# Performance work log

Measured on AMD Instinct MI355X. Metric: run time of the kernel, lower is better.

The kernel has to match this reference:

```python
import jax, jax.numpy as jnp
import numpy as np

EPS = 1e-5

def _bn_train(x, gamma, beta):
    # BatchNorm2d in training mode: batch stats over (N,H,W), biased variance
    mean = jnp.mean(x, axis=(0, 2, 3), keepdims=True)
    var = jnp.mean((x - mean) ** 2, axis=(0, 2, 3), keepdims=True)
    xn = (x - mean) / jnp.sqrt(var + EPS)
    return xn * gamma[None, :, None, None] + beta[None, :, None, None]

def _bin_act(x):
    # forward: sign(x); backward: grad of clamp(x,-1,1) (STE)
    c = jnp.clip(x, -1.0, 1.0)
    return jax.lax.stop_gradient(jnp.sign(x) - c) + c

def _bin_conv(x, w_flat, out_chn, in_chn, k=3, stride=1, padding=1):
    w = w_flat.reshape(out_chn, in_chn, k, k)
    scale = jax.lax.stop_gradient(jnp.mean(jnp.abs(w), axis=(1, 2, 3), keepdims=True))
    cw = jnp.clip(w, -1.0, 1.0)
    bw = jax.lax.stop_gradient(scale * jnp.sign(w) - cw) + cw
    return jax.lax.conv_general_dilated(
        x, bw, window_strides=(stride, stride),
        padding=[(padding, padding), (padding, padding)],
        dimension_numbers=('NCHW', 'OIHW', 'NCHW'))

def _prelu(x, a):
    return jnp.where(x >= 0, x, a * x)

def setup_inputs() -> dict:
    key = jax.random.key(0)
    ks = jax.random.split(key, 4)
    C = 128
    x = jax.random.normal(ks[0], (64, C, 56, 56), dtype=jnp.float32)
    # HardBinaryConv stores weights as (n,1); init small, mixed-sign
    w1 = (jax.random.uniform(ks[1], (C * C * 9, 1), dtype=jnp.float32) - 0.5) * 0.002
    w2 = (jax.random.uniform(ks[2], (C * C * 9, 1), dtype=jnp.float32) - 0.5) * 0.002
    ones = jnp.ones((C,), jnp.float32)
    zeros = jnp.zeros((C,), jnp.float32)
    a = jnp.float32(0.25)
    return {
        'x': x,
        'bn1_g': ones, 'bn1_b': zeros,
        'w1': w1, 'prelu1_a': a,
        'bn2_g': ones, 'bn2_b': zeros,
        'w2': w2, 'prelu2_a': a,
        'bn3_g': ones, 'bn3_b': zeros,
        'prelu3_a': a,
    }

def reference(x, bn1_g, bn1_b, w1, prelu1_a, bn2_g, bn2_b, w2, prelu2_a, bn3_g, bn3_b, prelu3_a):
    C = x.shape[1]
    out = _bn_train(x, bn1_g, bn1_b)
    out = _bin_act(out)
    out = _prelu(_bin_conv(out, w1, C, C), prelu1_a)
    out = _bn_train(out, bn2_g, bn2_b)
    out = _bin_act(out)
    out = _bin_conv(out, w2, C, C)
    out = _prelu(out, prelu2_a)
    out = _bn_train(out, bn3_g, bn3_b)
    out = out + x  # identity shortcut (stride=1, in_planes==planes)
    out = _prelu(out, prelu3_a)
    return out
```

## Files before the change

kernel.cpp:

```cpp
#include <hip/hip_runtime.h>
#include <hip/hip_bf16.h>

typedef __attribute__((ext_vector_type(8))) short short8;
typedef __attribute__((ext_vector_type(4))) int i32x4;

#define HW     3136
#define M_TOT  200704
#define NSTEP  18
#define NBLK   1568

__device__ __forceinline__ void gload_lds16(const void* g, void* l) {
    __builtin_amdgcn_global_load_lds(
        (const __attribute__((address_space(1))) void*)g,
        (__attribute__((address_space(3))) void*)l, 16, 0, 0);
}

__global__ __launch_bounds__(256) void wsign_kernel(const float* __restrict__ w1,
                                                    const float* __restrict__ w2,
                                                    char* __restrict__ ws1,
                                                    char* __restrict__ ws2) {
    int i = blockIdx.x * 256 + threadIdx.x;
    const float* w = w1;
    char* wsz = ws1;
    if (i >= 147456) { i -= 147456; w = w2; wsz = ws2; }
    int e = i & 15, l = (i >> 4) & 63, f = (i >> 10) & 7, s = i >> 13;
    int cout = f * 16 + (l & 15);
    int k = s * 64 + (l >> 4) * 16 + e;
    int tap = k >> 7, cin = k & 127;
    float v = w[(cout * 128 + cin) * 9 + tap];
    wsz[i] = v > 0.f ? (char)1 : (v < 0.f ? (char)-1 : (char)0);
}

__global__ __launch_bounds__(256) void wscale_kernel(const float* __restrict__ w1,
                                                     const float* __restrict__ w2,
                                                     float* __restrict__ scale1,
                                                     float* __restrict__ scale2) {
    int o = blockIdx.x;
    const float* w = w1;
    float* scale = scale1;
    if (o >= 128) { o -= 128; w = w2; scale = scale2; }
    int t = threadIdx.x;
    float s = 0.f;
    for (int i = t; i < 1152; i += 256) s += fabsf(w[o * 1152 + i]);
    __shared__ float r1[256];
    r1[t] = s; __syncthreads();
    for (int off = 128; off > 0; off >>= 1) {
        if (t < off) r1[t] += r1[t + off];
        __syncthreads();
    }
    if (t == 0) scale[o] = r1[0] * (1.f / 1152.f);
}

__global__ __launch_bounds__(256) void stats_nchw_kernel(const float* __restrict__ x,
                                                         float* __restrict__ psum,
                                                         float* __restrict__ psq) {
    int bid = blockIdx.x;
    int n = bid >> 7, c = bid & 127;
    const float* p = x + (n * 128 + c) * HW;
    int t = threadIdx.x;
    float s = 0.f, q = 0.f;
    for (int i = t; i < HW; i += 256) { float v = p[i]; s += v; q += v * v; }
    __shared__ float r1[256], r2[256];
    r1[t] = s; r2[t] = q; __syncthreads();
    for (int off = 128; off > 0; off >>= 1) {
        if (t < off) { r1[t] += r1[t + off]; r2[t] += r2[t + off]; }
        __syncthreads();
    }
    if (t == 0) { psum[c * 64 + n] = r1[0]; psq[c * 64 + n] = r2[0]; }
}

__global__ void finalize_kernel(const float* __restrict__ psum, const float* __restrict__ psq,
                                int P, float* __restrict__ mean, float* __restrict__ rstd) {
    int c = threadIdx.x;
    if (c >= 128) return;
    float s = 0.f, q = 0.f;
    for (int j = 0; j < P; ++j) { s += psum[c * P + j]; q += psq[c * P + j]; }
    const float invN = 1.f / 200704.f;
    float m = s * invN;
    float var = q * invN - m * m;
    mean[c] = m;
    rstd[c] = 1.f / sqrtf(var + 1e-5f);
}

__global__ __launch_bounds__(256) void finalizeB_kernel(const float* __restrict__ psumB,
                                                        const float* __restrict__ psqB,
                                                        float* __restrict__ mean,
                                                        float* __restrict__ rstd) {
    int c = blockIdx.x, t = threadIdx.x;
    float s = 0.f, q = 0.f;
    for (int j = t; j < NBLK; j += 256) { s += psumB[c * NBLK + j]; q += psqB[c * NBLK + j]; }
    __shared__ float r1[256], r2[256];
    r1[t] = s; r2[t] = q; __syncthreads();
    for (int off = 128; off > 0; off >>= 1) {
        if (t < off) { r1[t] += r1[t + off]; r2[t] += r2[t + off]; }
        __syncthreads();
    }
    if (t == 0) {
        const float invN = 1.f / 200704.f;
        float m = r1[0] * invN;
        float var = r2[0] * invN - m * m;
        mean[c] = m;
        rstd[c] = 1.f / sqrtf(var + 1e-5f);
    }
}

__global__ __launch_bounds__(256) void act1_kernel(const float* __restrict__ x,
        const float* __restrict__ mean, const float* __restrict__ rstd,
        const float* __restrict__ g, const float* __restrict__ b,
        char* __restrict__ apad) {
    __shared__ float row[128 * 57];
    int blk = blockIdx.x;
    int n = blk / 58, hp = blk - n * 58;
    char* o = apad + (n * 58 + hp) * 58 * 128;
    int t = threadIdx.x;
    if (hp == 0 || hp == 57) {
        for (int i4 = t; i4 < 58 * 32; i4 += 256)
            *(char4*)(o + i4 * 4) = make_char4(0, 0, 0, 0);
        return;
    }
    const float* src = x + n * (128 * HW) + (hp - 1) * 56;
    for (int i = t; i < 128 * 56; i += 256) {
        int c = i / 56, w = i - c * 56;
        row[c * 57 + w] = src[c * HW + w];
    }
    __syncthreads();
    for (int i4 = t; i4 < 58 * 32; i4 += 256) {
        int wp = i4 >> 5;
        int c0 = (i4 & 31) * 4;
        char q[4] = {0, 0, 0, 0};
        if (wp >= 1 && wp <= 56) {
#pragma unroll
            for (int k = 0; k < 4; ++k) {
                int c = c0 + k;
                float xn = (row[c * 57 + wp - 1] - mean[c]) * rstd[c] * g[c] + b[c];
                q[k] = xn > 0.f ? 1 : (xn < 0.f ? -1 : 0);
            }
        }
        *(char4*)(o + wp * 128 + c0) = make_char4(q[0], q[1], q[2], q[3]);
    }
}

__global__ __launch_bounds__(256) void act2_kernel(const short* __restrict__ p1,
        const float* __restrict__ scale1, const float* __restrict__ a1ptr,
        const float* __restrict__ mean, const float* __restrict__ rstd,
        const float* __restrict__ g, const float* __restrict__ b,
        char* __restrict__ apad) {
    __shared__ float row[128 * 57];
    int blk = blockIdx.x;
    int n = blk / 58, hp = blk - n * 58;
    char* o = apad + (n * 58 + hp) * 58 * 128;
    int t = threadIdx.x;
    if (hp == 0 || hp == 57) {
        for (int i4 = t; i4 < 58 * 32; i4 += 256)
            *(char4*)(o + i4 * 4) = make_char4(0, 0, 0, 0);
        return;
    }
    float a1 = a1ptr[0];
    const short* src = p1 + n * HW + (hp - 1) * 56;
    for (int i = t; i < 128 * 56; i += 256) {
        int c = i / 56, w = i - c * 56;
        float v = scale1[c] * (float)src[(size_t)c * M_TOT + w];
        row[c * 57 + w] = v >= 0.f ? v : a1 * v;
    }
    __syncthreads();
    for (int i4 = t; i4 < 58 * 32; i4 += 256) {
        int wp = i4 >> 5;
        int c0 = (i4 & 31) * 4;
        char q[4] = {0, 0, 0, 0};
        if (wp >= 1 && wp <= 56) {
#pragma unroll
            for (int k = 0; k < 4; ++k) {
                int c = c0 + k;
                float xn = (row[c * 57 + wp - 1] - mean[c]) * rstd[c] * g[c] + b[c];
                q[k] = xn > 0.f ? 1 : (xn < 0.f ? -1 : 0);
            }
        }
        *(char4*)(o + wp * 128 + c0) = make_char4(q[0], q[1], q[2], q[3]);
    }
}

__global__ __launch_bounds__(256, 3) void conv_kernel(
        const char* __restrict__ apad,
        const char* __restrict__ wswz,
        const float* __restrict__ scale,
        const float* __restrict__ aptr,
        short* __restrict__ obuf,
        float* __restrict__ psumB,
        float* __restrict__ psqB) {
    __shared__ __align__(1024) char lds[3][16384];

    const int tid = threadIdx.x;
    const int lane = tid & 63;
    const int wid = tid >> 6;
    const int l15 = lane & 15;
    const int lq = lane >> 4;
    const int wr = wid >> 1;
    const int wc = wid & 1;

    int bid = blockIdx.x;
    int mblk = (bid & 7) * 196 + (bid >> 3);
    const int m0 = mblk * 128;

    const char* bsrc[2];
#pragma unroll
    for (int j = 0; j < 2; ++j) {
        int m = m0 + (j * 4 + wid) * 16 + l15;
        int n = m / HW;
        int r = m - n * HW;
        int h = r / 56;
        int w = r - h * 56;
        bsrc[j] = apad + (((n * 58 + h) * 58 + w) * 128 + lq * 16);
    }

    i32x4 acc[4][4];
#pragma unroll
    for (int i = 0; i < 4; ++i)
#pragma unroll
        for (int j = 0; j < 4; ++j)
            acc[i][j] = (i32x4){0, 0, 0, 0};

    auto stage = [&](int s, int buf) {
        int tap = s >> 1;
        int dh = tap / 3;
        int dw = tap - dh * 3;
        int toff = (dh * 58 + dw) * 128 + (s & 1) * 64;
        const char* wsrc = wswz + s * 8192 + tid * 16;
        gload_lds16(wsrc,        lds[buf] + wid * 1024);
        gload_lds16(wsrc + 4096, lds[buf] + 4096 + wid * 1024);
        gload_lds16(bsrc[0] + toff, lds[buf] + 8192 + wid * 1024);
        gload_lds16(bsrc[1] + toff, lds[buf] + 8192 + 4096 + wid * 1024);
    };

    stage(0, 0);
    stage(1, 1);

    for (int s = 0; s < NSTEP; ++s) {
        if (s + 1 < NSTEP) asm volatile("s_waitcnt vmcnt(4)" ::: "memory");
        else               asm volatile("s_waitcnt vmcnt(0)" ::: "memory");
        __builtin_amdgcn_s_barrier();
        __builtin_amdgcn_sched_barrier(0);
        if (s + 2 < NSTEP) stage(s + 2, (s + 2) % 3);

        const char* buf = lds[s % 3];
        i32x4 af[4], bf[4];
#pragma unroll
        for (int ci = 0; ci < 4; ++ci)
            af[ci] = *(const i32x4*)(buf + (wr * 4 + ci) * 1024 + lane * 16);
#pragma unroll
        for (int mi = 0; mi < 4; ++mi)
            bf[mi] = *(const i32x4*)(buf + 8192 + (wc * 4 + mi) * 1024 + lane * 16);
#pragma unroll
        for (int ci = 0; ci < 4; ++ci)
#pragma unroll
            for (int mi = 0; mi < 4; ++mi)
                acc[ci][mi] = __builtin_amdgcn_mfma_i32_16x16x64_i8(
                    af[ci], bf[mi], acc[ci][mi], 0, 0, 0);
    }

    float alpha = aptr[0];
    float* partS = (float*)&lds[0][0];
    float* partQ = (float*)&lds[0][1024];
#pragma unroll
    for (int ci = 0; ci < 4; ++ci) {
        int cb = wr * 64 + ci * 16 + lq * 4;
        int mb = m0 + wc * 64 + l15;
#pragma unroll
        for (int r = 0; r < 4; ++r) {
            float sc = scale[cb + r];
            short* op = obuf + (size_t)(cb + r) * M_TOT + mb;
            float s = 0.f, q = 0.f;
#pragma unroll
            for (int mi = 0; mi < 4; ++mi) {
                int iv = acc[ci][mi][r];
                float v = (float)iv * sc;
                float pv = v >= 0.f ? v : alpha * v;
                op[mi * 16] = (short)iv;
                s += pv; q += pv * pv;
            }
#pragma unroll
            for (int msk = 1; msk <= 8; msk <<= 1) {
                s += __shfl_xor(s, msk, 64);
                q += __shfl_xor(q, msk, 64);
            }
            if (l15 == 0) { partS[wc * 128 + cb + r] = s; partQ[wc * 128 + cb + r] = q; }
        }
    }
    __syncthreads();
    if (tid < 128) {
        psumB[tid * NBLK + bid] = partS[tid] + partS[128 + tid];
        psqB [tid * NBLK + bid] = partQ[tid] + partQ[128 + tid];
    }
}

__global__ __launch_bounds__(256) void final_kernel(const short* __restrict__ p2,
        const float* __restrict__ scale2, const float* __restrict__ a2ptr,
        const float* __restrict__ x,
        const float* __restrict__ mean, const float* __restrict__ rstd,
        const float* __restrict__ g, const float* __restrict__ b,
        const float* __restrict__ a3ptr, float* __restrict__ out) {
    int bid = blockIdx.x;
    int n = bid >> 7, c = bid & 127;
    float sc = scale2[c], a2 = a2ptr[0];
    float m = mean[c], r = rstd[c], gg = g[c], bb = b[c], a3 = a3ptr[0];
    const short* pp = p2 + (size_t)c * M_TOT + n * HW;
    const float* xx = x + (n * 128 + c) * HW;
    float* oo = out + (n * 128 + c) * HW;
    int t = threadIdx.x;
    for (int i8 = t; i8 < 392; i8 += 256) {
        short8 v = *(const short8*)(pp + i8 * 8);
        float4 x0 = *(const float4*)(xx + i8 * 8);
        float4 x1 = *(const float4*)(xx + i8 * 8 + 4);
        float o[8];
#pragma unroll
        for (int k = 0; k < 8; ++k) {
            float pv = (float)v[k] * sc;
            pv = pv >= 0.f ? pv : a2 * pv;
            float xv = (k < 4) ? ((const float*)&x0)[k] : ((const float*)&x1)[k - 4];
            float val = (pv - m) * r * gg + bb + xv;
            o[k] = val >= 0.f ? val : a3 * val;
        }
        *(float4*)(oo + i8 * 8)     = make_float4(o[0], o[1], o[2], o[3]);
        *(float4*)(oo + i8 * 8 + 4) = make_float4(o[4], o[5], o[6], o[7]);
    }
}

extern "C" void kernel_launch(void* const* d_in, const int* in_sizes, int n_in,
                              void* d_out, int out_size, void* d_ws, size_t ws_size,
                              hipStream_t stream) {
    const float* x  = (const float*)d_in[0];
    const float* g1 = (const float*)d_in[1];
    const float* b1 = (const float*)d_in[2];
    const float* w1 = (const float*)d_in[3];
    const float* a1 = (const float*)d_in[4];
    const float* g2 = (const float*)d_in[5];
    const float* b2 = (const float*)d_in[6];
    const float* w2 = (const float*)d_in[7];
    const float* a2 = (const float*)d_in[8];
    const float* g3 = (const float*)d_in[9];
    const float* b3 = (const float*)d_in[10];
    const float* a3 = (const float*)d_in[11];
    float* out = (float*)d_out;
    char* ws = (char*)d_ws;

    float* scale1 = (float*)(ws);
    float* scale2 = (float*)(ws + 512);
    float* mean1  = (float*)(ws + 1024);
    float* rstd1  = (float*)(ws + 1536);
    float* mean2  = (float*)(ws + 2048);
    float* rstd2  = (float*)(ws + 2560);
    float* mean3  = (float*)(ws + 3072);
    float* rstd3  = (float*)(ws + 3584);
    float* psum   = (float*)(ws + 4096);
    float* psq    = (float*)(ws + 36864);
    float* psumB  = (float*)(ws + 69632);
    float* psqB   = (float*)(ws + 872448);
    char* wswz1   = (char*)(ws + 1675264);
    char* wswz2   = (char*)(ws + 1822720);
    char* apad8   = (char*)(ws + 1970176);
    short* buf2s  = (short*)(ws + 29528064);
    short* buf1s  = (short*)out;

    wscale_kernel<<<256, 256, 0, stream>>>(w1, w2, scale1, scale2);
    wsign_kernel<<<1152, 256, 0, stream>>>(w1, w2, wswz1, wswz2);

    stats_nchw_kernel<<<8192, 256, 0, stream>>>(x, psum, psq);
    finalize_kernel<<<1, 128, 0, stream>>>(psum, psq, 64, mean1, rstd1);
    act1_kernel<<<3712, 256, 0, stream>>>(x, mean1, rstd1, g1, b1, apad8);
    conv_kernel<<<1568, 256, 0, stream>>>(apad8, wswz1, scale1, a1, buf1s, psumB, psqB);

    finalizeB_kernel<<<128, 256, 0, stream>>>(psumB, psqB, mean2, rstd2);
    act2_kernel<<<3712, 256, 0, stream>>>(buf1s, scale1, a1, mean2, rstd2, g2, b2, apad8);
    conv_kernel<<<1568, 256, 0, stream>>>(apad8, wswz2, scale2, a2, buf2s, psumB, psqB);

    finalizeB_kernel<<<128, 256, 0, stream>>>(psumB, psqB, mean3, rstd3);
    final_kernel<<<8192, 256, 0, stream>>>(buf2s, scale2, a2, x, mean3, rstd3, g3, b3, a3, out);
}
```

Measured before the change: 275.0 us.

## Double conv M-tile to 256 rows per block to reuse weight tiles

Each conv block now covers 256 output pixels instead of 128, so every staged weight slice feeds twice as many MFMAs and the per-block accumulators grow to 4x8. LDS per stage rises to 24KB, the grid halves to 784 blocks, and occupancy drops to 2 blocks per CU. The partial-stat layout is transposed to [block][channel] and the finalize reads are changed to match. Doubling the accumulators raises register pressure, and the smaller grid gives fewer waves to hide latency.

```diff
diff --git a/kernel.cpp b/kernel.cpp
--- a/kernel.cpp
+++ b/kernel.cpp
@@ -7,7 +7,7 @@
 #define HW     3136
 #define M_TOT  200704
 #define NSTEP  18
-#define NBLK   1568
+#define NBLK   784
 
 __device__ __forceinline__ void gload_lds16(const void* g, void* l) {
     __builtin_amdgcn_global_load_lds(
@@ -88,7 +88,7 @@
                                                         float* __restrict__ rstd) {
     int c = blockIdx.x, t = threadIdx.x;
     float s = 0.f, q = 0.f;
-    for (int j = t; j < NBLK; j += 256) { s += psumB[c * NBLK + j]; q += psqB[c * NBLK + j]; }
+    for (int j = t; j < NBLK; j += 256) { s += psumB[j * 128 + c]; q += psqB[j * 128 + c]; }
     __shared__ float r1[256], r2[256];
     r1[t] = s; r2[t] = q; __syncthreads();
     for (int off = 128; off > 0; off >>= 1) {
@@ -179,7 +179,7 @@
     }
 }
 
-__global__ __launch_bounds__(256, 3) void conv_kernel(
+__global__ __launch_bounds__(256, 2) void conv_kernel(
         const char* __restrict__ apad,
         const char* __restrict__ wswz,
         const float* __restrict__ scale,
@@ -187,7 +187,7 @@
         short* __restrict__ obuf,
         float* __restrict__ psumB,
         float* __restrict__ psqB) {
-    __shared__ __align__(1024) char lds[3][16384];
+    __shared__ __align__(1024) char lds[3][24576];
 
     const int tid = threadIdx.x;
     const int lane = tid & 63;
@@ -198,13 +198,14 @@
     const int wc = wid & 1;
 
     int bid = blockIdx.x;
-    int mblk = (bid & 7) * 196 + (bid >> 3);
-    const int m0 = mblk * 128;
-
-    const char* bsrc[2];
-#pragma unroll
-    for (int j = 0; j < 2; ++j) {
-        int m = m0 + (j * 4 + wid) * 16 + l15;
+    int mblk = (bid & 7) * 98 + (bid >> 3);
+    const int m0 = mblk * 256;
+
+    const char* bsrc[4];
+#pragma unroll
+    for (int j = 0; j < 4; ++j) {
+        int jt = j >> 1, jj = j & 1;
+        int m = m0 + jt * 128 + (jj * 4 + wid) * 16 + l15;
         int n = m / HW;
         int r = m - n * HW;
         int h = r / 56;
@@ -212,11 +213,11 @@
         bsrc[j] = apad + (((n * 58 + h) * 58 + w) * 128 + lq * 16);
     }
 
-    i32x4 acc[4][4];
+    i32x4 acc[4][8];
 #pragma unroll
     for (int i = 0; i < 4; ++i)
 #pragma unroll
-        for (int j = 0; j < 4; ++j)
+        for (int j = 0; j < 8; ++j)
             acc[i][j] = (i32x4){0, 0, 0, 0};
 
     auto stage = [&](int s, int buf) {
@@ -228,33 +229,38 @@
         gload_lds16(wsrc,        lds[buf] + wid * 1024);
         gload_lds16(wsrc + 4096, lds[buf] + 4096 + wid * 1024);
         gload_lds16(bsrc[0] + toff, lds[buf] + 8192 + wid * 1024);
-        gload_lds16(bsrc[1] + toff, lds[buf] + 8192 + 4096 + wid * 1024);
+        gload_lds16(bsrc[1] + toff, lds[buf] + 12288 + wid * 1024);
+        gload_lds16(bsrc[2] + toff, lds[buf] + 16384 + wid * 1024);
+        gload_lds16(bsrc[3] + toff, lds[buf] + 20480 + wid * 1024);
     };
 
     stage(0, 0);
     stage(1, 1);
 
     for (int s = 0; s < NSTEP; ++s) {
-        if (s + 1 < NSTEP) asm volatile("s_waitcnt vmcnt(4)" ::: "memory");
+        if (s + 1 < NSTEP) asm volatile("s_waitcnt vmcnt(6)" ::: "memory");
         else               asm volatile("s_waitcnt vmcnt(0)" ::: "memory");
         __builtin_amdgcn_s_barrier();
         __builtin_amdgcn_sched_barrier(0);
         if (s + 2 < NSTEP) stage(s + 2, (s + 2) % 3);
 
         const char* buf = lds[s % 3];
-        i32x4 af[4], bf[4];
+        i32x4 af[4], bf[8];
 #pragma unroll
         for (int ci = 0; ci < 4; ++ci)
             af[ci] = *(const i32x4*)(buf + (wr * 4 + ci) * 1024 + lane * 16);
 #pragma unroll
-        for (int mi = 0; mi < 4; ++mi)
-            bf[mi] = *(const i32x4*)(buf + 8192 + (wc * 4 + mi) * 1024 + lane * 16);
+        for (int t2 = 0; t2 < 2; ++t2)
+#pragma unroll
+            for (int mi = 0; mi < 4; ++mi)
+                bf[t2 * 4 + mi] = *(const i32x4*)(buf + 8192 + t2 * 8192 +
+                                                  (wc * 4 + mi) * 1024 + lane * 16);
 #pragma unroll
         for (int ci = 0; ci < 4; ++ci)
 #pragma unroll
-            for (int mi = 0; mi < 4; ++mi)
-                acc[ci][mi] = __builtin_amdgcn_mfma_i32_16x16x64_i8(
-                    af[ci], bf[mi], acc[ci][mi], 0, 0, 0);
+            for (int j = 0; j < 8; ++j)
+                acc[ci][j] = __builtin_amdgcn_mfma_i32_16x16x64_i8(
+                    af[ci], bf[j], acc[ci][j], 0, 0, 0);
     }
 
     float alpha = aptr[0];
@@ -263,19 +269,22 @@
 #pragma unroll
     for (int ci = 0; ci < 4; ++ci) {
         int cb = wr * 64 + ci * 16 + lq * 4;
-        int mb = m0 + wc * 64 + l15;
 #pragma unroll
         for (int r = 0; r < 4; ++r) {
             float sc = scale[cb + r];
-            short* op = obuf + (size_t)(cb + r) * M_TOT + mb;
             float s = 0.f, q = 0.f;
 #pragma unroll
-            for (int mi = 0; mi < 4; ++mi) {
-                int iv = acc[ci][mi][r];
-                float v = (float)iv * sc;
-                float pv = v >= 0.f ? v : alpha * v;
-                op[mi * 16] = (short)iv;
-                s += pv; q += pv * pv;
+            for (int t2 = 0; t2 < 2; ++t2) {
+                int mb = m0 + t2 * 128 + wc * 64 + l15;
+                short* op = obuf + (size_t)(cb + r) * M_TOT + mb;
+#pragma unroll
+                for (int mi = 0; mi < 4; ++mi) {
+                    int iv = acc[ci][t2 * 4 + mi][r];
+                    float v = (float)iv * sc;
+                    float pv = v >= 0.f ? v : alpha * v;
+                    op[mi * 16] = (short)iv;
+                    s += pv; q += pv * pv;
+                }
             }
 #pragma unroll
             for (int msk = 1; msk <= 8; msk <<= 1) {
@@ -287,8 +296,8 @@
     }
     __syncthreads();
     if (tid < 128) {
-        psumB[tid * NBLK + bid] = partS[tid] + partS[128 + tid];
-        psqB [tid * NBLK + bid] = partQ[tid] + partQ[128 + tid];
+        psumB[bid * 128 + tid] = partS[tid] + partS[128 + tid];
+        psqB [bid * 128 + tid] = partQ[tid] + partQ[128 + tid];
     }
 }
 
@@ -366,11 +375,11 @@
     stats_nchw_kernel<<<8192, 256, 0, stream>>>(x, psum, psq);
     finalize_kernel<<<1, 128, 0, stream>>>(psum, psq, 64, mean1, rstd1);
     act1_kernel<<<3712, 256, 0, stream>>>(x, mean1, rstd1, g1, b1, apad8);
-    conv_kernel<<<1568, 256, 0, stream>>>(apad8, wswz1, scale1, a1, buf1s, psumB, psqB);
+    conv_kernel<<<NBLK, 256, 0, stream>>>(apad8, wswz1, scale1, a1, buf1s, psumB, psqB);
 
     finalizeB_kernel<<<128, 256, 0, stream>>>(psumB, psqB, mean2, rstd2);
     act2_kernel<<<3712, 256, 0, stream>>>(buf1s, scale1, a1, mean2, rstd2, g2, b2, apad8);
-    conv_kernel<<<1568, 256, 0, stream>>>(apad8, wswz2, scale2, a2, buf2s, psumB, psqB);
+    conv_kernel<<<NBLK, 256, 0, stream>>>(apad8, wswz2, scale2, a2, buf2s, psumB, psqB);
 
     finalizeB_kernel<<<128, 256, 0, stream>>>(psumB, psqB, mean3, rstd3);
     final_kernel<<<8192, 256, 0, stream>>>(buf2s, scale2, a2, x, mean3, rstd3, g3, b3, a3, out);
```

Measured after the change: 274.4 us. Within noise of the previous version (-0.2%).
